# Kernel optimization log

Measured on AMD Instinct MI355X. Metric: run time of the kernel, lower is better.

The kernel has to match this reference:

```python
import jax, jax.numpy as jnp
import numpy as np

N_NODES = 50000
N_EDGES = 800000
D_NODE = 64
D_EDGE = 32
D_OUT = 64


def setup_inputs() -> dict:
    key = jax.random.key(0)
    ks = jax.random.split(key, 8)
    node_feats = jax.random.normal(ks[0], (N_NODES, D_NODE), dtype=jnp.float32)
    edge_feats = jax.random.normal(ks[1], (N_EDGES, D_EDGE), dtype=jnp.float32)
    src = jax.random.randint(ks[2], (N_EDGES,), 0, N_NODES, dtype=jnp.int32)
    dst = jax.random.randint(ks[3], (N_EDGES,), 0, N_NODES, dtype=jnp.int32)
    # f_e: Linear(D_NODE + D_EDGE + D_NODE -> D_OUT), f_v: Linear(D_OUT + D_NODE -> D_OUT)
    d_in_e = D_NODE + D_EDGE + D_NODE
    d_in_v = D_OUT + D_NODE
    W_e = jax.random.normal(ks[4], (d_in_e, D_OUT), dtype=jnp.float32) / np.sqrt(d_in_e)
    b_e = jnp.zeros((D_OUT,), dtype=jnp.float32)
    W_v = jax.random.normal(ks[5], (d_in_v, D_OUT), dtype=jnp.float32) / np.sqrt(d_in_v)
    b_v = jnp.zeros((D_OUT,), dtype=jnp.float32)
    return {"node_feats": node_feats, "edge_feats": edge_feats, "src": src, "dst": dst,
            "W_e": W_e, "b_e": b_e, "W_v": W_v, "b_v": b_v}


def reference(node_feats, edge_feats, src, dst, W_e, b_e, W_v, b_v):
    n_nodes = node_feats.shape[0]
    # Edge update: gather src/dst node feats, concat with edge feats, MLP + ReLU
    x_e = jnp.concatenate([node_feats[src], edge_feats, node_feats[dst]], axis=1)  # [E, 2*Dn+De]
    m = jax.nn.relu(x_e @ W_e + b_e)  # [E, D_OUT]
    # Mean aggregation by destination node (DGL 'mean': 0 for isolated nodes)
    msum = jax.ops.segment_sum(m, dst, num_segments=n_nodes)  # [N, D_OUT]
    deg = jax.ops.segment_sum(jnp.ones((dst.shape[0],), dtype=m.dtype), dst, num_segments=n_nodes)
    neigh = jnp.where(deg[:, None] > 0, msum / jnp.maximum(deg[:, None], 1.0), 0.0)
    # Node update MLP
    x_v = jnp.concatenate([neigh, node_feats], axis=1)  # [N, D_OUT + Dn]
    return jax.nn.relu(x_v @ W_v + b_v)
```

## Files before the change

### kernel.cpp

```cpp
#include <hip/hip_runtime.h>

#define DN 64
#define DE 32
#define DO 64
#define NB 256
#define TP 128
#define CH 8

typedef __attribute__((ext_vector_type(8))) short bf16x8;
typedef __attribute__((ext_vector_type(4))) float f32x4;

__device__ inline unsigned pack_bf16(float a, float b) {
    unsigned ua = __float_as_uint(a), ub = __float_as_uint(b);
    ua = (ua + 0x7fffu + ((ua >> 16) & 1u)) >> 16;
    ub = (ub + 0x7fffu + ((ub >> 16) & 1u)) >> 16;
    return ua | (ub << 16);
}
__device__ inline unsigned short bf16_1(float a) {
    unsigned u = __float_as_uint(a);
    return (unsigned short)((u + 0x7fffu + ((u >> 16) & 1u)) >> 16);
}
__device__ inline float bf16f(unsigned short v) {
    return __uint_as_float((unsigned)v << 16);
}

union bfu { unsigned u[4]; bf16x8 v; };

__global__ void __launch_bounds__(256) pre_hist_kernel(
    const float* __restrict__ node, const float* __restrict__ W_e,
    const int* __restrict__ dst,
    unsigned short* __restrict__ PsB, unsigned short* __restrict__ PdB,
    int* __restrict__ cnt, int n_nodes, int n_edges)
{
    const int t    = threadIdx.x;
    const int lane = t & 63;
    const int w    = __builtin_amdgcn_readfirstlane((int)(t >> 6));
    const int l15  = lane & 15;
    const int k0   = (lane >> 4) << 3;

    bfu bS[4][2], bD[4][2];
#pragma unroll
    for (int Nt = 0; Nt < 4; ++Nt) {
        const int col = (Nt << 4) | l15;
#pragma unroll
        for (int ks = 0; ks < 2; ++ks) {
            float ws[8], wd[8];
#pragma unroll
            for (int e = 0; e < 8; ++e) {
                ws[e] = W_e[(ks * 32 + k0 + e) * DO + col];
                wd[e] = W_e[(96 + ks * 32 + k0 + e) * DO + col];
            }
#pragma unroll
            for (int q = 0; q < 4; ++q) {
                bS[Nt][ks].u[q] = pack_bf16(ws[2 * q], ws[2 * q + 1]);
                bD[Nt][ks].u[q] = pack_bf16(wd[2 * q], wd[2 * q + 1]);
            }
        }
    }

    const int row0 = blockIdx.x * 64 + w * 16;
    if (row0 < n_nodes) {
        bfu aF[2];
#pragma unroll
        for (int ks = 0; ks < 2; ++ks) {
            const int r = min(row0 + l15, n_nodes - 1);
            const float* __restrict__ p = node + (size_t)r * DN + ks * 32 + k0;
            const float4 f0 = *(const float4*)p;
            const float4 f1 = *(const float4*)(p + 4);
            aF[ks].u[0] = pack_bf16(f0.x, f0.y);
            aF[ks].u[1] = pack_bf16(f0.z, f0.w);
            aF[ks].u[2] = pack_bf16(f1.x, f1.y);
            aF[ks].u[3] = pack_bf16(f1.z, f1.w);
        }
        const int rb = row0 + ((lane >> 4) << 2);
#pragma unroll
        for (int Nt = 0; Nt < 4; ++Nt) {
            const f32x4 z = {0.f, 0.f, 0.f, 0.f};
            f32x4 aS = __builtin_amdgcn_mfma_f32_16x16x32_bf16(aF[0].v, bS[Nt][0].v, z, 0, 0, 0);
            aS = __builtin_amdgcn_mfma_f32_16x16x32_bf16(aF[1].v, bS[Nt][1].v, aS, 0, 0, 0);
            f32x4 aD = __builtin_amdgcn_mfma_f32_16x16x32_bf16(aF[0].v, bD[Nt][0].v, z, 0, 0, 0);
            aD = __builtin_amdgcn_mfma_f32_16x16x32_bf16(aF[1].v, bD[Nt][1].v, aD, 0, 0, 0);
            const int col = (Nt << 4) | l15;
#pragma unroll
            for (int r = 0; r < 4; ++r) {
                if (rb + r < n_nodes) {
                    PsB[(size_t)(rb + r) * DO + col] = bf16_1(aS[r]);
                    PdB[(size_t)(rb + r) * DO + col] = bf16_1(aD[r]);
                }
            }
        }
    }

    const int gt = blockIdx.x * blockDim.x + t;
    const int nt = gridDim.x * blockDim.x;
    for (int e = gt; e < n_edges; e += nt)
        atomicAdd(&cnt[dst[e]], 1);
}

__global__ void __launch_bounds__(256) scan_partial(
    const int* __restrict__ cnt, int* __restrict__ local,
    int* __restrict__ bsum, int n_nodes)
{
    const int C = (n_nodes + NB - 1) / NB;
    const int t = threadIdx.x, lane = t & 63, w = t >> 6;
    const int i = blockIdx.x * C + t;

    int v = (t < C && i < n_nodes) ? cnt[i] : 0;
    int incl = v;
#pragma unroll
    for (int off = 1; off < 64; off <<= 1) {
        int u = __shfl_up(incl, off, 64);
        if (lane >= off) incl += u;
    }
    __shared__ int ws[4], wo[4];
    if (lane == 63) ws[w] = incl;
    __syncthreads();
    if (t == 0) {
        int r = 0;
#pragma unroll
        for (int q = 0; q < 4; ++q) { wo[q] = r; r += ws[q]; }
        bsum[blockIdx.x] = r;
    }
    __syncthreads();
    if (t < C && i < n_nodes) local[i] = incl - v + wo[w];
}

__global__ void __launch_bounds__(256) scan_final(
    const int* __restrict__ local, const int* __restrict__ bsum,
    int* __restrict__ row_start, int* __restrict__ cursor, int n_nodes)
{
    const int t = threadIdx.x, lane = t & 63, w = t >> 6;
    int v = bsum[t];
    int incl = v;
#pragma unroll
    for (int off = 1; off < 64; off <<= 1) {
        int u = __shfl_up(incl, off, 64);
        if (lane >= off) incl += u;
    }
    __shared__ int ws[4], wo[4];
    if (lane == 63) ws[w] = incl;
    __syncthreads();
    if (t == 0) {
        int r = 0;
#pragma unroll
        for (int q = 0; q < 4; ++q) { wo[q] = r; r += ws[q]; }
    }
    __syncthreads();
    const int excl = incl - v + wo[w];

    __shared__ int blockoff;
    if (t == (int)blockIdx.x) blockoff = excl;
    if (blockIdx.x == NB - 1 && t == NB - 1) row_start[n_nodes] = excl + v;
    __syncthreads();

    const int C = (n_nodes + NB - 1) / NB;
    const int i = blockIdx.x * C + t;
    if (t < C && i < n_nodes) {
        int r = local[i] + blockoff;
        row_start[i] = r;
        cursor[i]    = r;
    }
}

__global__ void __launch_bounds__(256) scatter_kernel(
    const int* __restrict__ dst, const int* __restrict__ src,
    int* __restrict__ cursor, int2* __restrict__ csr, int n_edges)
{
    const int half = (n_edges + 1) >> 1;
    const int g = blockIdx.x * blockDim.x + threadIdx.x;
    if (g >= half) return;
    const int e1 = g + half;
    const bool h1 = e1 < n_edges;
    const int d0 = dst[g];
    const int s0 = src[g];
    const int d1 = h1 ? dst[e1] : 0;
    const int s1 = h1 ? src[e1] : 0;
    const int p0 = atomicAdd(&cursor[d0], 1);
    const int p1 = h1 ? atomicAdd(&cursor[d1], 1) : 0;
    csr[p0] = make_int2(g, s0 | (d0 << 16));
    if (h1) csr[p1] = make_int2(e1, s1 | (d1 << 16));
}

__global__ void __launch_bounds__(128) agg_mfma_kernel(
    const float* __restrict__ edge,
    const float* __restrict__ W_e, const float* __restrict__ b_e,
    const unsigned short* __restrict__ PsB, const unsigned short* __restrict__ PdB,
    const int* __restrict__ row_start, const int2* __restrict__ csr,
    float* __restrict__ msum, int n_edges)
{
    __shared__ unsigned lds_m[2][32][68];

    const int t    = threadIdx.x;
    const int lane = t & 63;
    const int wid  = __builtin_amdgcn_readfirstlane((int)(t >> 6));
    const int wbeg = blockIdx.x * TP + wid * 64;
    const int wcnt = min(n_edges - wbeg, 64);
    if (wcnt <= 0) return;

    const int l15 = lane & 15;
    const int k0  = (lane >> 4) << 3;

    bfu bfr[4];
#pragma unroll
    for (int Nt = 0; Nt < 4; ++Nt) {
        const int col = (Nt << 4) | l15;
        float wv[8];
#pragma unroll
        for (int e = 0; e < 8; ++e)
            wv[e] = W_e[(64 + k0 + e) * DO + col];
#pragma unroll
        for (int v2 = 0; v2 < 4; ++v2)
            bfr[Nt].u[v2] = pack_bf16(wv[2 * v2], wv[2 * v2 + 1]);
    }
    const float bj = b_e[lane];

    const int2 my2 = csr[min(wbeg + lane, n_edges - 1)];

#pragma unroll
    for (int Mt = 0; Mt < 4; ++Mt) {
        const int eA = __shfl(my2.x, (Mt << 4) | l15, 64);
        const float* __restrict__ ep = edge + (size_t)(unsigned)eA * DE + k0;
        const float4 f0 = *(const float4*)(ep);
        const float4 f1 = *(const float4*)(ep + 4);
        bfu afr;
        afr.u[0] = pack_bf16(f0.x, f0.y);
        afr.u[1] = pack_bf16(f0.z, f0.w);
        afr.u[2] = pack_bf16(f1.x, f1.y);
        afr.u[3] = pack_bf16(f1.z, f1.w);
        const int rp0 = (Mt << 3) + ((lane >> 4) << 1);
#pragma unroll
        for (int Nt = 0; Nt < 4; ++Nt) {
            f32x4 dz = {0.f, 0.f, 0.f, 0.f};
            f32x4 d = __builtin_amdgcn_mfma_f32_16x16x32_bf16(afr.v, bfr[Nt].v, dz, 0, 0, 0);
            const int col = (Nt << 4) | l15;
            lds_m[wid][rp0][col]     = pack_bf16(d[0], d[1]);
            lds_m[wid][rp0 + 1][col] = pack_bf16(d[2], d[3]);
        }
    }

    float acc = 0.f, bpd = 0.f;
    int cur_d = -1;

#define FLUSH()                                                         \
    {                                                                   \
        if (row_start[cur_d] >= wbeg)                                   \
            msum[(size_t)cur_d * DO + lane] = acc;                      \
        else                                                            \
            unsafeAtomicAdd(&msum[(size_t)cur_d * DO + lane], acc);     \
    }

#define ISSUE(CHK, BUF)                                                 \
    _Pragma("unroll")                                                   \
    for (int q = 0; q < CH; ++q) {                                      \
        const int y = __builtin_amdgcn_readlane(my2.y, (CHK) * CH + q); \
        BUF[q] = PsB[(size_t)(unsigned)(y & 0xffff) * DO + lane];       \
    }

#define CONSUME(CHK, BUF)                                               \
    {                                                                   \
        unsigned um[4];                                                 \
        _Pragma("unroll")                                               \
        for (int h = 0; h < 4; ++h)                                     \
            um[h] = lds_m[wid][(CHK) * 4 + h][lane];                    \
        _Pragma("unroll")                                               \
        for (int q = 0; q < CH; ++q) {                                  \
            const int y = __builtin_amdgcn_readlane(my2.y, (CHK) * CH + q); \
            const int d = (int)(((unsigned)y) >> 16);                   \
            if (d != cur_d) {                                           \
                if (cur_d >= 0) FLUSH();                                \
                acc = 0.f;                                              \
                cur_d = d;                                              \
                bpd = bj + bf16f(PdB[(size_t)(unsigned)d * DO + lane]); \
            }                                                           \
            const unsigned u = um[q >> 1];                              \
            const float mv = (q & 1) ? __uint_as_float(u & 0xffff0000u) \
                                     : __uint_as_float(u << 16);        \
            acc += fmaxf(mv + bpd + __uint_as_float((unsigned)BUF[q] << 16), 0.f); \
        }                                                               \
    }

    if (wcnt == 64) {
        unsigned short pnA[CH], pnB[CH], pnC[CH];
        ISSUE(0, pnA) ISSUE(1, pnB)
        ISSUE(2, pnC) CONSUME(0, pnA)
        ISSUE(3, pnA) CONSUME(1, pnB)
        ISSUE(4, pnB) CONSUME(2, pnC)
        ISSUE(5, pnC) CONSUME(3, pnA)
        ISSUE(6, pnA) CONSUME(4, pnB)
        ISSUE(7, pnB) CONSUME(5, pnC)
        CONSUME(6, pnA)
        CONSUME(7, pnB)
    } else {
        for (int p = 0; p < wcnt; ++p) {
            const int y = __builtin_amdgcn_readlane(my2.y, p);
            const int s = y & 0xffff;
            const int d = (int)(((unsigned)y) >> 16);
            const float ps = bf16f(PsB[(size_t)(unsigned)s * DO + lane]);
            if (d != cur_d) {
                if (cur_d >= 0) FLUSH();
                acc = 0.f;
                cur_d = d;
                bpd = bj + bf16f(PdB[(size_t)(unsigned)d * DO + lane]);
            }
            const unsigned u = lds_m[wid][p >> 1][lane];
            const float mv = (p & 1) ? __uint_as_float(u & 0xffff0000u)
                                     : __uint_as_float(u << 16);
            acc += fmaxf(mv + bpd + ps, 0.f);
        }
    }

    {
        const int sb = row_start[cur_d];
        const int se = row_start[cur_d + 1];
        if (sb >= wbeg && se <= wbeg + wcnt)
            msum[(size_t)cur_d * DO + lane] = acc;
        else
            unsafeAtomicAdd(&msum[(size_t)cur_d * DO + lane], acc);
    }
#undef FLUSH
#undef ISSUE
#undef CONSUME
}

__global__ void __launch_bounds__(256) node_out_kernel(
    const float* __restrict__ node, const float* __restrict__ msum,
    const int* __restrict__ row_start,
    const float* __restrict__ W_v, const float* __restrict__ b_v,
    float* __restrict__ out, int n_nodes)
{
    const int t    = threadIdx.x;
    const int lane = t & 63;
    const int w    = __builtin_amdgcn_readfirstlane((int)(t >> 6));
    const int l15  = lane & 15;
    const int k0   = (lane >> 4) << 3;

    bfu bT[4][2], bB[4][2];
#pragma unroll
    for (int Nt = 0; Nt < 4; ++Nt) {
        const int col = (Nt << 4) | l15;
#pragma unroll
        for (int ks = 0; ks < 2; ++ks) {
            float wt[8], wb[8];
#pragma unroll
            for (int e = 0; e < 8; ++e) {
                wt[e] = W_v[(ks * 32 + k0 + e) * DO + col];
                wb[e] = W_v[(64 + ks * 32 + k0 + e) * DO + col];
            }
#pragma unroll
            for (int q = 0; q < 4; ++q) {
                bT[Nt][ks].u[q] = pack_bf16(wt[2 * q], wt[2 * q + 1]);
                bB[Nt][ks].u[q] = pack_bf16(wb[2 * q], wb[2 * q + 1]);
            }
        }
    }

    const int row0 = blockIdx.x * 64 + w * 16;
    if (row0 >= n_nodes) return;

    bfu aM[2], aN[2];
#pragma unroll
    for (int ks = 0; ks < 2; ++ks) {
        const int r = min(row0 + l15, n_nodes - 1);
        const float* __restrict__ pm = msum + (size_t)r * DO + ks * 32 + k0;
        const float* __restrict__ pn = node + (size_t)r * DN + ks * 32 + k0;
        const float4 m0 = *(const float4*)pm;
        const float4 m1 = *(const float4*)(pm + 4);
        const float4 n0 = *(const float4*)pn;
        const float4 n1 = *(const float4*)(pn + 4);
        aM[ks].u[0] = pack_bf16(m0.x, m0.y);
        aM[ks].u[1] = pack_bf16(m0.z, m0.w);
        aM[ks].u[2] = pack_bf16(m1.x, m1.y);
        aM[ks].u[3] = pack_bf16(m1.z, m1.w);
        aN[ks].u[0] = pack_bf16(n0.x, n0.y);
        aN[ks].u[1] = pack_bf16(n0.z, n0.w);
        aN[ks].u[2] = pack_bf16(n1.x, n1.y);
        aN[ks].u[3] = pack_bf16(n1.z, n1.w);
    }

    f32x4 accT[4], accB[4];
#pragma unroll
    for (int Nt = 0; Nt < 4; ++Nt) {
        const f32x4 z = {0.f, 0.f, 0.f, 0.f};
        f32x4 aT = __builtin_amdgcn_mfma_f32_16x16x32_bf16(aM[0].v, bT[Nt][0].v, z, 0, 0, 0);
        aT = __builtin_amdgcn_mfma_f32_16x16x32_bf16(aM[1].v, bT[Nt][1].v, aT, 0, 0, 0);
        f32x4 aB = __builtin_amdgcn_mfma_f32_16x16x32_bf16(aN[0].v, bB[Nt][0].v, z, 0, 0, 0);
        aB = __builtin_amdgcn_mfma_f32_16x16x32_bf16(aN[1].v, bB[Nt][1].v, aB, 0, 0, 0);
        accT[Nt] = aT;
        accB[Nt] = aB;
    }

    const int rb = row0 + ((lane >> 4) << 2);
#pragma unroll
    for (int r = 0; r < 4; ++r) {
        const int row = rb + r;
        if (row < n_nodes) {
            const float dg = (float)(row_start[row + 1] - row_start[row]);
            const float inv = (dg > 0.f) ? 1.f / dg : 0.f;
#pragma unroll
            for (int Nt = 0; Nt < 4; ++Nt) {
                const int col = (Nt << 4) | l15;
                const float val = accT[Nt][r] * inv + accB[Nt][r] + b_v[col];
                out[(size_t)row * DO + col] = fmaxf(val, 0.f);
            }
        }
    }
}

extern "C" void kernel_launch(void* const* d_in, const int* in_sizes, int n_in,
                              void* d_out, int out_size, void* d_ws, size_t ws_size,
                              hipStream_t stream)
{
    const float* node = (const float*)d_in[0];
    const float* edge = (const float*)d_in[1];
    const int*   src  = (const int*)d_in[2];
    const int*   dst  = (const int*)d_in[3];
    const float* W_e  = (const float*)d_in[4];
    const float* b_e  = (const float*)d_in[5];
    const float* W_v  = (const float*)d_in[6];
    const float* b_v  = (const float*)d_in[7];
    float* out = (float*)d_out;

    const int n_nodes = in_sizes[0] / DN;
    const int n_edges = in_sizes[2];
    const int ntiles  = (n_nodes + 63) / 64;

    unsigned short* PsB = (unsigned short*)d_ws;
    unsigned short* PdB = PsB + (size_t)n_nodes * DO;
    float* msum = (float*)(PdB + (size_t)n_nodes * DO);
    int* cnt       = (int*)(msum + (size_t)n_nodes * DO);
    int* row_start = cnt + n_nodes;
    int* cursor    = row_start + (n_nodes + 1);
    int* local     = cursor + n_nodes;
    int* bsum      = local + n_nodes;
    int2* csr      = (int2*)(((size_t)(bsum + NB) + 15) & ~(size_t)15);

    hipMemsetAsync(msum, 0, ((size_t)n_nodes * DO + n_nodes) * sizeof(float), stream);

    pre_hist_kernel<<<ntiles, 256, 0, stream>>>(node, W_e, dst, PsB, PdB, cnt,
                                                n_nodes, n_edges);
    scan_partial<<<NB, 256, 0, stream>>>(cnt, local, bsum, n_nodes);
    scan_final<<<NB, 256, 0, stream>>>(local, bsum, row_start, cursor, n_nodes);
    scatter_kernel<<<((n_edges + 1) / 2 + 255) / 256, 256, 0, stream>>>(dst, src, cursor, csr, n_edges);
    agg_mfma_kernel<<<(n_edges + TP - 1) / TP, 128, 0, stream>>>(edge, W_e, b_e, PsB, PdB,
                                                                 row_start, csr, msum, n_edges);
    node_out_kernel<<<ntiles, 256, 0, stream>>>(node, msum, row_start, W_v, b_v,
                                                out, n_nodes);
}
```

Baseline: 163.9 us.

## Merge scan and scatter into one cooperative kernel with rank-based CSR placement

The histogram pass now stores each edge's atomic rank, so the scatter step can compute CSR positions as row_start plus rank and no longer needs atomics or a cursor array. The two scan kernels and the scatter are fused into a single cooperative kernel separated by grid-wide syncs, removing two kernel launches. In exchange, every edge writes and later reads an extra rank array, and the cooperative launch with 1024 blocks must fit co-resident, with grid.sync adding its own overhead. CSR order within each node now follows atomic order from the histogram pass.

```diff
diff --git a/kernel.cpp b/kernel.cpp
--- a/kernel.cpp
+++ b/kernel.cpp
@@ -1,4 +1,7 @@
 #include <hip/hip_runtime.h>
+#include <hip/hip_cooperative_groups.h>
+
+namespace cg = cooperative_groups;
 
 #define DN 64
 #define DE 32
@@ -6,6 +9,7 @@
 #define NB 256
 #define TP 128
 #define CH 8
+#define COOPB 1024
 
 typedef __attribute__((ext_vector_type(8))) short bf16x8;
 typedef __attribute__((ext_vector_type(4))) float f32x4;
@@ -30,7 +34,8 @@
     const float* __restrict__ node, const float* __restrict__ W_e,
     const int* __restrict__ dst,
     unsigned short* __restrict__ PsB, unsigned short* __restrict__ PdB,
-    int* __restrict__ cnt, int n_nodes, int n_edges)
+    int* __restrict__ cnt, int* __restrict__ rank_,
+    int n_nodes, int n_edges)
 {
     const int t    = threadIdx.x;
     const int lane = t & 63;
@@ -94,91 +99,76 @@
     const int gt = blockIdx.x * blockDim.x + t;
     const int nt = gridDim.x * blockDim.x;
     for (int e = gt; e < n_edges; e += nt)
-        atomicAdd(&cnt[dst[e]], 1);
-}
-
-__global__ void __launch_bounds__(256) scan_partial(
-    const int* __restrict__ cnt, int* __restrict__ local,
-    int* __restrict__ bsum, int n_nodes)
+        rank_[e] = atomicAdd(&cnt[dst[e]], 1);
+}
+
+__global__ void __launch_bounds__(256) csr_coop_kernel(
+    const int* __restrict__ dst, const int* __restrict__ src,
+    const int* __restrict__ rank_, const int* __restrict__ cnt,
+    int* __restrict__ local, int* __restrict__ bsum,
+    int* __restrict__ row_start, int2* __restrict__ csr,
+    int n_nodes, int n_edges)
 {
+    cg::grid_group grid = cg::this_grid();
+    __shared__ int ws[4], wo[4], blockoff;
+
+    const int t = threadIdx.x, lane = t & 63, w = t >> 6;
     const int C = (n_nodes + NB - 1) / NB;
-    const int t = threadIdx.x, lane = t & 63, w = t >> 6;
-    const int i = blockIdx.x * C + t;
-
-    int v = (t < C && i < n_nodes) ? cnt[i] : 0;
-    int incl = v;
-#pragma unroll
-    for (int off = 1; off < 64; off <<= 1) {
-        int u = __shfl_up(incl, off, 64);
-        if (lane >= off) incl += u;
-    }
-    __shared__ int ws[4], wo[4];
-    if (lane == 63) ws[w] = incl;
-    __syncthreads();
-    if (t == 0) {
-        int r = 0;
-#pragma unroll
-        for (int q = 0; q < 4; ++q) { wo[q] = r; r += ws[q]; }
-        bsum[blockIdx.x] = r;
-    }
-    __syncthreads();
-    if (t < C && i < n_nodes) local[i] = incl - v + wo[w];
-}
-
-__global__ void __launch_bounds__(256) scan_final(
-    const int* __restrict__ local, const int* __restrict__ bsum,
-    int* __restrict__ row_start, int* __restrict__ cursor, int n_nodes)
-{
-    const int t = threadIdx.x, lane = t & 63, w = t >> 6;
-    int v = bsum[t];
-    int incl = v;
-#pragma unroll
-    for (int off = 1; off < 64; off <<= 1) {
-        int u = __shfl_up(incl, off, 64);
-        if (lane >= off) incl += u;
-    }
-    __shared__ int ws[4], wo[4];
-    if (lane == 63) ws[w] = incl;
-    __syncthreads();
-    if (t == 0) {
-        int r = 0;
-#pragma unroll
-        for (int q = 0; q < 4; ++q) { wo[q] = r; r += ws[q]; }
-    }
-    __syncthreads();
-    const int excl = incl - v + wo[w];
-
-    __shared__ int blockoff;
-    if (t == (int)blockIdx.x) blockoff = excl;
-    if (blockIdx.x == NB - 1 && t == NB - 1) row_start[n_nodes] = excl + v;
-    __syncthreads();
-
-    const int C = (n_nodes + NB - 1) / NB;
-    const int i = blockIdx.x * C + t;
-    if (t < C && i < n_nodes) {
-        int r = local[i] + blockoff;
-        row_start[i] = r;
-        cursor[i]    = r;
-    }
-}
-
-__global__ void __launch_bounds__(256) scatter_kernel(
-    const int* __restrict__ dst, const int* __restrict__ src,
-    int* __restrict__ cursor, int2* __restrict__ csr, int n_edges)
-{
-    const int half = (n_edges + 1) >> 1;
-    const int g = blockIdx.x * blockDim.x + threadIdx.x;
-    if (g >= half) return;
-    const int e1 = g + half;
-    const bool h1 = e1 < n_edges;
-    const int d0 = dst[g];
-    const int s0 = src[g];
-    const int d1 = h1 ? dst[e1] : 0;
-    const int s1 = h1 ? src[e1] : 0;
-    const int p0 = atomicAdd(&cursor[d0], 1);
-    const int p1 = h1 ? atomicAdd(&cursor[d1], 1) : 0;
-    csr[p0] = make_int2(g, s0 | (d0 << 16));
-    if (h1) csr[p1] = make_int2(e1, s1 | (d1 << 16));
+
+    if (blockIdx.x < NB) {
+        const int i = blockIdx.x * C + t;
+        int v = (t < C && i < n_nodes) ? cnt[i] : 0;
+        int incl = v;
+#pragma unroll
+        for (int off = 1; off < 64; off <<= 1) {
+            int u = __shfl_up(incl, off, 64);
+            if (lane >= off) incl += u;
+        }
+        if (lane == 63) ws[w] = incl;
+        __syncthreads();
+        if (t == 0) {
+            int r = 0;
+#pragma unroll
+            for (int q = 0; q < 4; ++q) { wo[q] = r; r += ws[q]; }
+            bsum[blockIdx.x] = r;
+        }
+        __syncthreads();
+        if (t < C && i < n_nodes) local[i] = incl - v + wo[w];
+    }
+    grid.sync();
+
+    if (blockIdx.x < NB) {
+        int v = bsum[t];
+        int incl = v;
+#pragma unroll
+        for (int off = 1; off < 64; off <<= 1) {
+            int u = __shfl_up(incl, off, 64);
+            if (lane >= off) incl += u;
+        }
+        if (lane == 63) ws[w] = incl;
+        __syncthreads();
+        if (t == 0) {
+            int r = 0;
+#pragma unroll
+            for (int q = 0; q < 4; ++q) { wo[q] = r; r += ws[q]; }
+        }
+        __syncthreads();
+        const int excl = incl - v + wo[w];
+        if (t == (int)blockIdx.x) blockoff = excl;
+        if (blockIdx.x == NB - 1 && t == NB - 1) row_start[n_nodes] = excl + v;
+        __syncthreads();
+        const int i = blockIdx.x * C + t;
+        if (t < C && i < n_nodes) row_start[i] = local[i] + blockoff;
+    }
+    grid.sync();
+
+    const int gt = blockIdx.x * blockDim.x + t;
+    const int nt = gridDim.x * blockDim.x;
+    for (int e = gt; e < n_edges; e += nt) {
+        const int d = dst[e];
+        const int p = row_start[d] + rank_[e];
+        csr[p] = make_int2(e, src[e] | (d << 16));
+    }
 }
 
 __global__ void __launch_bounds__(128) agg_mfma_kernel(
@@ -420,8 +410,8 @@
     const float* b_v  = (const float*)d_in[7];
     float* out = (float*)d_out;
 
-    const int n_nodes = in_sizes[0] / DN;
-    const int n_edges = in_sizes[2];
+    int n_nodes = in_sizes[0] / DN;
+    int n_edges = in_sizes[2];
     const int ntiles  = (n_nodes + 63) / 64;
 
     unsigned short* PsB = (unsigned short*)d_ws;
@@ -429,18 +419,24 @@
     float* msum = (float*)(PdB + (size_t)n_nodes * DO);
     int* cnt       = (int*)(msum + (size_t)n_nodes * DO);
     int* row_start = cnt + n_nodes;
-    int* cursor    = row_start + (n_nodes + 1);
-    int* local     = cursor + n_nodes;
+    int* local     = row_start + (n_nodes + 1);
     int* bsum      = local + n_nodes;
-    int2* csr      = (int2*)(((size_t)(bsum + NB) + 15) & ~(size_t)15);
+    int* rank_     = bsum + NB;
+    int2* csr      = (int2*)(((size_t)(rank_ + n_edges) + 15) & ~(size_t)15);
 
     hipMemsetAsync(msum, 0, ((size_t)n_nodes * DO + n_nodes) * sizeof(float), stream);
 
-    pre_hist_kernel<<<ntiles, 256, 0, stream>>>(node, W_e, dst, PsB, PdB, cnt,
-                                                n_nodes, n_edges);
-    scan_partial<<<NB, 256, 0, stream>>>(cnt, local, bsum, n_nodes);
-    scan_final<<<NB, 256, 0, stream>>>(local, bsum, row_start, cursor, n_nodes);
-    scatter_kernel<<<((n_edges + 1) / 2 + 255) / 256, 256, 0, stream>>>(dst, src, cursor, csr, n_edges);
+    pre_hist_kernel<<<ntiles, 256, 0, stream>>>(node, W_e, dst, PsB, PdB,
+                                                cnt, rank_, n_nodes, n_edges);
+
+    {
+        void* args[] = { (void*)&dst, (void*)&src, (void*)&rank_, (void*)&cnt,
+                         (void*)&local, (void*)&bsum, (void*)&row_start,
+                         (void*)&csr, (void*)&n_nodes, (void*)&n_edges };
+        hipLaunchCooperativeKernel((const void*)csr_coop_kernel,
+                                   dim3(COOPB), dim3(256), args, 0, stream);
+    }
+
     agg_mfma_kernel<<<(n_edges + TP - 1) / TP, 128, 0, stream>>>(edge, W_e, b_e, PsB, PdB,
                                                                  row_start, csr, msum, n_edges);
     node_out_kernel<<<ntiles, 256, 0, stream>>>(node, msum, row_start, W_v, b_v,
```

Measured after the change: 358.4 us. +118.7%, slower.
